# Performance work log

Hardware: AMD Instinct MI355X
Metric: run time of the kernel (lower is better)

The kernel has to match this reference:

```python
import jax, jax.numpy as jnp
import numpy as np

B, TQ, TK = 64, 1, 2048
QD, KD, U, H = 512, 512, 1024, 8
D = U // H  # per-head dim = 128


def setup_inputs() -> dict:
    key0 = jax.random.key(0)
    k0, k1, k2, k3, k4 = jax.random.split(key0, 5)
    query = jax.random.normal(k0, (B, TQ, QD), jnp.float32)
    key = jax.random.normal(k1, (B, TK, KD), jnp.float32)
    # 1x1 Conv1d == Linear: weight [out_ch, in_ch], bias [out_ch]
    Wq = jax.random.normal(k2, (U, QD), jnp.float32) / np.sqrt(QD).astype(np.float32)
    bq = jnp.zeros((U,), jnp.float32)
    Wk = jax.random.normal(k3, (U, KD), jnp.float32) / np.sqrt(KD).astype(np.float32)
    bk = jnp.zeros((U,), jnp.float32)
    # v is generated with torch.randn every forward in the original (unlearned);
    # here it is a fixed random vector of size D (per-head units).
    v = jax.random.normal(k4, (D,), jnp.float32)
    return {"query": query, "key": key, "Wq": Wq, "bq": bq, "Wk": Wk, "bk": bk, "v": v}


def reference(query, key, Wq, bq, Wk, bk, v):
    # 1x1 conv projections (channels-last linear)
    q = jnp.einsum('btq,uq->btu', query, Wq) + bq          # [B,TQ,U]
    k = jnp.einsum('btk,uk->btu', key, Wk) + bk            # [B,TK,U]
    # split heads: torch.stack(torch.split(x, D, dim=2), dim=1) -> [B,H,T,D]
    qs = q.reshape(B, TQ, H, D).transpose(0, 2, 1, 3)      # [B,H,TQ,D]
    ks = k.reshape(B, TK, H, D).transpose(0, 2, 1, 3)      # [B,H,TK,D]
    # weight-normalized random projection vector (b is zeros, folded away)
    g = np.float32(1.0) / np.sqrt(D).astype(np.float32)
    normed_v = g * v * jax.lax.rsqrt(jnp.sum(v * v))       # [D]
    # additive score: sum_d normed_v * tanh(ks + qs)  (qs broadcasts over TK)
    add = jnp.einsum('d,bhtd->bht', normed_v, jnp.tanh(ks + qs))  # [B,H,TK]
    # F.softmax without dim on a 4D tensor -> legacy dim=1 (heads axis)
    weights = jax.nn.softmax(add[:, :, None, :], axis=1)   # [B,H,TQ,TK]
    # value = unprojected key, shared across heads
    context = jnp.einsum('bhqt,btd->bhqd', weights, key)   # [B,H,TQ,KD]
    # view(B, TQ, -1): valid because TQ == 1
    return context.reshape(B, TQ, H * KD)
```

## Files before the change

kernel.cpp:

```cpp
#include <hip/hip_runtime.h>

#define B_   64
#define TK_  2048
#define KD_  512
#define U_   1024
#define H_   8
#define D_   128
#define MT   64
#define NTILE (TK_ / MT)
#define GRID (B_ * NTILE)

typedef float f32x4 __attribute__((ext_vector_type(4)));
typedef short short8 __attribute__((ext_vector_type(8)));

__device__ __forceinline__ short f2bf(float f) {
    unsigned u = __float_as_uint(f);
    u += 0x7fffu + ((u >> 16) & 1u);
    return (short)(u >> 16);
}
__device__ __forceinline__ float bf2f(short s) {
    return __uint_as_float(((unsigned)(unsigned short)s) << 16);
}
__device__ __forceinline__ float tanh_fast(float x) {
    float e = __builtin_amdgcn_exp2f(x * 2.885390081777927f);
    return 1.0f - 2.0f * __builtin_amdgcn_rcpf(1.0f + e);
}

__device__ __forceinline__ void wg_barrier_lds() {
    asm volatile("" ::: "memory");
    __builtin_amdgcn_s_waitcnt(0xC07F);
    __builtin_amdgcn_s_barrier();
    asm volatile("" ::: "memory");
}

__device__ __forceinline__ void write_frag(short* As, int t, int c4, float4 v) {
    int ks = c4 >> 5;
    int lq = (c4 >> 3) & 3;
    int E  = ((lq << 4) | (t & 15)) ^ (ks & 7);
    int si = ((ks * 4 + (t >> 4)) << 9) + (E << 3) + (c4 & 4);
    short4 h4;
    h4.x = f2bf(v.x); h4.y = f2bf(v.y); h4.z = f2bf(v.z); h4.w = f2bf(v.w);
    *(short4*)&As[si] = h4;
}

__global__ void nv_kernel(const float* __restrict__ v, float* __restrict__ wsNV) {
    __shared__ float red[D_];
    int tid = threadIdx.x;
    float x = v[tid];
    red[tid] = x * x;
    __syncthreads();
    if (tid == 0) {
        float s = 0.f;
        for (int i = 0; i < D_; ++i) s += red[i];
        red[0] = rsqrtf(s) * 0.08838834764831845f;
    }
    __syncthreads();
    wsNV[tid] = x * red[0];
}

__global__ void q_kernel(const float* __restrict__ query, const float* __restrict__ Wq,
                         const float* __restrict__ bq, const float* __restrict__ bk,
                         float* __restrict__ wsQ) {
    __shared__ float qrow[KD_];
    int b = blockIdx.x, ug = blockIdx.y, tid = threadIdx.x;
    if (tid < 128) ((float4*)qrow)[tid] = ((const float4*)(query + (size_t)b * KD_))[tid];
    __syncthreads();
    int u = ug * 256 + tid;
    const float4* wq = (const float4*)(Wq + (size_t)u * KD_);
    const float4* q4 = (const float4*)qrow;
    float acc = 0.f;
#pragma unroll 8
    for (int i = 0; i < KD_ / 4; ++i) {
        float4 a = q4[i], w = wq[i];
        acc += a.x * w.x + a.y * w.y + a.z * w.z + a.w * w.w;
    }
    wsQ[(size_t)b * U_ + u] = acc + bq[u] + bk[u];
}

__global__ void swz_kernel(const float* __restrict__ Wk, short* __restrict__ wsB) {
    int g = blockIdx.x * 256 + threadIdx.x;
    int slot = g >> 6, l = g & 63;
    int ublk = slot >> 4, ks = slot & 15;
    int u = ublk * 16 + (l & 15);
    int k0 = ks * 32 + ((l >> 4) << 3);
    const float* src = Wk + (size_t)u * KD_ + k0;
    short8 o;
#pragma unroll
    for (int j = 0; j < 8; ++j) o[j] = f2bf(src[j]);
    *(short8*)(wsB + (size_t)g * 8) = o;
}

template <bool ATOMIC>
__global__ __launch_bounds__(256, 2) void attn_kernel(
    const float* __restrict__ key, const short* __restrict__ wsB,
    const float* __restrict__ wsQ, const float* __restrict__ wsNV,
    float* __restrict__ outp)
{
    __shared__ short As[MT * KD_];
    __shared__ float S[MT][H_];
    __shared__ float Wt[MT][H_];

    int bx = blockIdx.x;
    int b = bx & 63, tt = bx >> 6;
    int tid = threadIdx.x;
    int w = tid >> 6, l = tid & 63;
    int l15 = l & 15;

    const float4* kt = (const float4*)(key + ((size_t)b * TK_ + (size_t)tt * MT) * KD_);

    float4 h0v[16], h1v[16];
#pragma unroll
    for (int j = 0; j < 16; ++j) {
        int idx = tid + j * 256;
        h0v[j] = kt[((idx >> 6) << 7) + (idx & 63)];
    }
#pragma unroll
    for (int j = 0; j < 16; ++j) {
        int idx = tid + j * 256;
        h1v[j] = kt[((idx >> 6) << 7) + (idx & 63) + 64];
    }
#pragma unroll
    for (int j = 0; j < 16; ++j) {
        int idx = tid + j * 256;
        write_frag(As, idx >> 6, (idx & 63) << 2, h0v[j]);
    }
    wg_barrier_lds();

    const short8* bp = (const short8*)wsB;

    float ps[4][4];
    f32x4 acc[4][4];
    short8 bc[4], bn[4];
    int bbase_cur = 0;

    for (int p = 0; p < 4; ++p) {
        int c = p >> 1, nh = p & 1;
        int ub = c * 512 + w * 128 + nh * 64;
        int bbase = (ub >> 4) * 1024 + l;
        bbase_cur = bbase;

        if (nh == 0) {
#pragma unroll
            for (int mf = 0; mf < 4; ++mf)
#pragma unroll
                for (int r = 0; r < 4; ++r) ps[mf][r] = 0.f;
        }
#pragma unroll
        for (int mf = 0; mf < 4; ++mf)
#pragma unroll
            for (int nf = 0; nf < 4; ++nf) acc[mf][nf] = (f32x4){0.f, 0.f, 0.f, 0.f};

#pragma unroll
        for (int nf = 0; nf < 4; ++nf) bc[nf] = bp[bbase + nf * 1024];

        auto gemm_seg = [&](int ks0, int ks1) {
#pragma unroll 1
            for (int ks = ks0; ks < ks1; ++ks) {
                if (ks < 15) {
#pragma unroll
                    for (int nf = 0; nf < 4; ++nf)
                        bn[nf] = bp[bbase_cur + nf * 1024 + (ks + 1) * 64];
                }
                int ab = ((ks * 4) << 9) + ((l ^ (ks & 7)) << 3);
                short8 a[4];
#pragma unroll
                for (int mf = 0; mf < 4; ++mf)
                    a[mf] = *(const short8*)&As[ab + (mf << 9)];
#pragma unroll
                for (int mf = 0; mf < 4; ++mf)
#pragma unroll
                    for (int nf = 0; nf < 4; ++nf)
                        acc[mf][nf] = __builtin_amdgcn_mfma_f32_16x16x32_bf16(
                            a[mf], bc[nf], acc[mf][nf], 0, 0, 0);
                if (ks < 15) {
#pragma unroll
                    for (int nf = 0; nf < 4; ++nf) bc[nf] = bn[nf];
                }
            }
        };

        if (p == 0) {
            gemm_seg(0, 8);
#pragma unroll
            for (int j = 0; j < 16; ++j) {
                int idx = tid + j * 256;
                write_frag(As, idx >> 6, ((idx & 63) << 2) + 256, h1v[j]);
            }
            wg_barrier_lds();
            gemm_seg(8, 16);
        } else {
            gemm_seg(0, 16);
        }

        float qv[4], nv[4];
#pragma unroll
        for (int nf = 0; nf < 4; ++nf) {
            qv[nf] = wsQ[(size_t)b * U_ + ub + nf * 16 + l15];
            nv[nf] = wsNV[nh * 64 + nf * 16 + l15];
        }
#pragma unroll
        for (int mf = 0; mf < 4; ++mf)
#pragma unroll
            for (int r = 0; r < 4; ++r) {
                float pp = ps[mf][r];
#pragma unroll
                for (int nf = 0; nf < 4; ++nf)
                    pp += nv[nf] * tanh_fast(acc[mf][nf][r] + qv[nf]);
                ps[mf][r] = pp;
            }
        if (nh == 1) {
            int h = c * 4 + w;
#pragma unroll
            for (int mf = 0; mf < 4; ++mf)
#pragma unroll
                for (int r = 0; r < 4; ++r) {
                    float pp = ps[mf][r];
                    pp += __shfl_xor(pp, 1);
                    pp += __shfl_xor(pp, 2);
                    pp += __shfl_xor(pp, 4);
                    pp += __shfl_xor(pp, 8);
                    if (l15 == 0) S[mf * 16 + (l >> 4) * 4 + r][h] = pp;
                }
        }
    }
    wg_barrier_lds();

    if (tid < MT) {
        float sv[H_];
        float mx = -1e30f;
#pragma unroll
        for (int h = 0; h < H_; ++h) { sv[h] = S[tid][h]; mx = fmaxf(mx, sv[h]); }
        float sum = 0.f;
#pragma unroll
        for (int h = 0; h < H_; ++h) {
            sv[h] = __builtin_amdgcn_exp2f((sv[h] - mx) * 1.4426950408889634f);
            sum += sv[h];
        }
        float inv = __builtin_amdgcn_rcpf(sum);
#pragma unroll
        for (int h = 0; h < H_; ++h) Wt[tid][h] = sv[h] * inv;
    }
    wg_barrier_lds();

    int dg8 = (tid & 63) << 3;
    int hp = tid >> 6;
    int vks = dg8 >> 5, vlq = (dg8 >> 3) & 3;
    float cacc[2][8] = {};
#pragma unroll 1
    for (int t = 0; t < MT; ++t) {
        int E = ((vlq << 4) | (t & 15)) ^ (vks & 7);
        short8 kk = *(const short8*)&As[((vks * 4 + (t >> 4)) << 9) + (E << 3)];
        float w0 = Wt[t][2 * hp], w1 = Wt[t][2 * hp + 1];
#pragma unroll
        for (int d = 0; d < 8; ++d) {
            float kv = bf2f(kk[d]);
            cacc[0][d] += w0 * kv;
            cacc[1][d] += w1 * kv;
        }
    }
    if (ATOMIC) {
        float* ob = outp + (size_t)b * (H_ * KD_);
#pragma unroll
        for (int j = 0; j < 2; ++j)
#pragma unroll
            for (int d = 0; d < 8; ++d)
                atomicAdd(&ob[(2 * hp + j) * KD_ + dg8 + d], cacc[j][d]);
    } else {
        float* pb = outp + (size_t)bx * (H_ * KD_);
#pragma unroll
        for (int j = 0; j < 2; ++j) {
            *(f32x4*)&pb[(2 * hp + j) * KD_ + dg8]     = *(f32x4*)&cacc[j][0];
            *(f32x4*)&pb[(2 * hp + j) * KD_ + dg8 + 4] = *(f32x4*)&cacc[j][4];
        }
    }
}

__global__ void reduce_kernel(const float* __restrict__ partial, float* __restrict__ out) {
    int o = blockIdx.x * 256 + threadIdx.x;
    int b = o >> 10;
    int u4 = o & 1023;
    const f32x4* p4 = (const f32x4*)partial;
    f32x4 s = {0.f, 0.f, 0.f, 0.f};
#pragma unroll 8
    for (int tt = 0; tt < NTILE; ++tt)
        s += p4[((size_t)(tt * 64 + b)) * 1024 + u4];
    ((f32x4*)out)[o] = s;
}

extern "C" void kernel_launch(void* const* d_in, const int* in_sizes, int n_in,
                              void* d_out, int out_size, void* d_ws, size_t ws_size,
                              hipStream_t stream) {
    const float* query = (const float*)d_in[0];
    const float* key   = (const float*)d_in[1];
    const float* Wq    = (const float*)d_in[2];
    const float* bq    = (const float*)d_in[3];
    const float* Wk    = (const float*)d_in[4];
    const float* bk    = (const float*)d_in[5];
    const float* v     = (const float*)d_in[6];
    float* out = (float*)d_out;

    char* ws = (char*)d_ws;
    float* wsNV = (float*)ws;
    float* wsQ  = (float*)(ws + 4096);
    short* wsB  = (short*)(ws + 524288);
    float* wsP  = (float*)(ws + 2 * 1024 * 1024);

    size_t need = 2 * 1024 * 1024 + (size_t)GRID * (H_ * KD_) * sizeof(float);

    nv_kernel<<<1, 128, 0, stream>>>(v, wsNV);
    q_kernel<<<dim3(64, 4), 256, 0, stream>>>(query, Wq, bq, bk, wsQ);
    swz_kernel<<<256, 256, 0, stream>>>(Wk, wsB);

    if (ws_size >= need) {
        attn_kernel<false><<<GRID, 256, 0, stream>>>(key, wsB, wsQ, wsNV, wsP);
        reduce_kernel<<<256, 256, 0, stream>>>(wsP, out);
    } else {
        hipMemsetAsync(d_out, 0, (size_t)out_size * sizeof(float), stream);
        attn_kernel<true><<<GRID, 256, 0, stream>>>(key, wsB, wsQ, wsNV, out);
    }
}
```

Before: 557.7 us.

## Use 512-thread blocks with one head per wave and padded LDS layout

Doubles the attention block to 8 waves so each wave owns one head's 128 projection units. The per-wave loop shrinks from four passes to two, cutting serial MFMA work per wave and raising occupancy. The swizzled LDS fragment layout is replaced by a row-major layout padded by 8 elements to limit bank conflicts, and the context accumulation now has each thread handle 4 columns. The trade-off is higher register pressure under launch_bounds(512,4) and possibly more LDS bank conflicts than the XOR swizzle had.

Measured after the change: 646.5 us. 1.16x slower.

```diff
diff --git a/kernel.cpp b/kernel.cpp
--- a/kernel.cpp
+++ b/kernel.cpp
@@ -7,6 +7,8 @@
 #define H_   8
 #define D_   128
 #define MT   64
+#define APAD 8
+#define ASTR (KD_ + APAD)
 #define NTILE (TK_ / MT)
 #define GRID (B_ * NTILE)
 
@@ -31,16 +33,6 @@
     __builtin_amdgcn_s_waitcnt(0xC07F);
     __builtin_amdgcn_s_barrier();
     asm volatile("" ::: "memory");
-}
-
-__device__ __forceinline__ void write_frag(short* As, int t, int c4, float4 v) {
-    int ks = c4 >> 5;
-    int lq = (c4 >> 3) & 3;
-    int E  = ((lq << 4) | (t & 15)) ^ (ks & 7);
-    int si = ((ks * 4 + (t >> 4)) << 9) + (E << 3) + (c4 & 4);
-    short4 h4;
-    h4.x = f2bf(v.x); h4.y = f2bf(v.y); h4.z = f2bf(v.z); h4.w = f2bf(v.w);
-    *(short4*)&As[si] = h4;
 }
 
 __global__ void nv_kernel(const float* __restrict__ v, float* __restrict__ wsNV) {
@@ -91,12 +83,12 @@
 }
 
 template <bool ATOMIC>
-__global__ __launch_bounds__(256, 2) void attn_kernel(
+__global__ __launch_bounds__(512, 4) void attn_kernel(
     const float* __restrict__ key, const short* __restrict__ wsB,
     const float* __restrict__ wsQ, const float* __restrict__ wsNV,
     float* __restrict__ outp)
 {
-    __shared__ short As[MT * KD_];
+    __shared__ short As[MT * ASTR];
     __shared__ float S[MT][H_];
     __shared__ float Wt[MT][H_];
 
@@ -104,25 +96,29 @@
     int b = bx & 63, tt = bx >> 6;
     int tid = threadIdx.x;
     int w = tid >> 6, l = tid & 63;
-    int l15 = l & 15;
+    int l15 = l & 15, lq = l >> 4;
 
     const float4* kt = (const float4*)(key + ((size_t)b * TK_ + (size_t)tt * MT) * KD_);
 
-    float4 h0v[16], h1v[16];
-#pragma unroll
-    for (int j = 0; j < 16; ++j) {
-        int idx = tid + j * 256;
+    float4 h0v[8], h1v[8];
+#pragma unroll
+    for (int j = 0; j < 8; ++j) {
+        int idx = tid + j * 512;
         h0v[j] = kt[((idx >> 6) << 7) + (idx & 63)];
     }
 #pragma unroll
-    for (int j = 0; j < 16; ++j) {
-        int idx = tid + j * 256;
+    for (int j = 0; j < 8; ++j) {
+        int idx = tid + j * 512;
         h1v[j] = kt[((idx >> 6) << 7) + (idx & 63) + 64];
     }
 #pragma unroll
-    for (int j = 0; j < 16; ++j) {
-        int idx = tid + j * 256;
-        write_frag(As, idx >> 6, (idx & 63) << 2, h0v[j]);
+    for (int j = 0; j < 8; ++j) {
+        int idx = tid + j * 512;
+        int t = idx >> 6, c4 = (idx & 63) << 2;
+        float4 v = h0v[j];
+        short4 h4;
+        h4.x = f2bf(v.x); h4.y = f2bf(v.y); h4.z = f2bf(v.z); h4.w = f2bf(v.w);
+        *(short4*)&As[t * ASTR + c4] = h4;
     }
     wg_barrier_lds();
 
@@ -133,22 +129,27 @@
     short8 bc[4], bn[4];
     int bbase_cur = 0;
 
-    for (int p = 0; p < 4; ++p) {
-        int c = p >> 1, nh = p & 1;
-        int ub = c * 512 + w * 128 + nh * 64;
+#pragma unroll
+    for (int mf = 0; mf < 4; ++mf)
+#pragma unroll
+        for (int r = 0; r < 4; ++r) ps[mf][r] = 0.f;
+
+    for (int p = 0; p < 2; ++p) {
+        int ub = w * 128 + p * 64;
         int bbase = (ub >> 4) * 1024 + l;
         bbase_cur = bbase;
 
-        if (nh == 0) {
-#pragma unroll
-            for (int mf = 0; mf < 4; ++mf)
-#pragma unroll
-                for (int r = 0; r < 4; ++r) ps[mf][r] = 0.f;
+#pragma unroll
+        for (int mf = 0; mf < 4; ++mf)
+#pragma unroll
+            for (int nf = 0; nf < 4; ++nf) acc[mf][nf] = (f32x4){0.f, 0.f, 0.f, 0.f};
+
+        float qv[4], nv[4];
+#pragma unroll
+        for (int nf = 0; nf < 4; ++nf) {
+            qv[nf] = wsQ[(size_t)b * U_ + ub + nf * 16 + l15];
+            nv[nf] = wsNV[p * 64 + nf * 16 + l15];
         }
-#pragma unroll
-        for (int mf = 0; mf < 4; ++mf)
-#pragma unroll
-            for (int nf = 0; nf < 4; ++nf) acc[mf][nf] = (f32x4){0.f, 0.f, 0.f, 0.f};
 
 #pragma unroll
         for (int nf = 0; nf < 4; ++nf) bc[nf] = bp[bbase + nf * 1024];
@@ -161,11 +162,10 @@
                     for (int nf = 0; nf < 4; ++nf)
                         bn[nf] = bp[bbase_cur + nf * 1024 + (ks + 1) * 64];
                 }
-                int ab = ((ks * 4) << 9) + ((l ^ (ks & 7)) << 3);
                 short8 a[4];
 #pragma unroll
                 for (int mf = 0; mf < 4; ++mf)
-                    a[mf] = *(const short8*)&As[ab + (mf << 9)];
+                    a[mf] = *(const short8*)&As[(mf * 16 + l15) * ASTR + ks * 32 + (lq << 3)];
 #pragma unroll
                 for (int mf = 0; mf < 4; ++mf)
 #pragma unroll
@@ -182,9 +182,13 @@
         if (p == 0) {
             gemm_seg(0, 8);
 #pragma unroll
-            for (int j = 0; j < 16; ++j) {
-                int idx = tid + j * 256;
-                write_frag(As, idx >> 6, ((idx & 63) << 2) + 256, h1v[j]);
+            for (int j = 0; j < 8; ++j) {
+                int idx = tid + j * 512;
+                int t = idx >> 6, c4 = ((idx & 63) << 2) + 256;
+                float4 v = h1v[j];
+                short4 h4;
+                h4.x = f2bf(v.x); h4.y = f2bf(v.y); h4.z = f2bf(v.z); h4.w = f2bf(v.w);
+                *(short4*)&As[t * ASTR + c4] = h4;
             }
             wg_barrier_lds();
             gemm_seg(8, 16);
@@ -192,12 +196,6 @@
             gemm_seg(0, 16);
         }
 
-        float qv[4], nv[4];
-#pragma unroll
-        for (int nf = 0; nf < 4; ++nf) {
-            qv[nf] = wsQ[(size_t)b * U_ + ub + nf * 16 + l15];
-            nv[nf] = wsNV[nh * 64 + nf * 16 + l15];
-        }
 #pragma unroll
         for (int mf = 0; mf < 4; ++mf)
 #pragma unroll
@@ -208,8 +206,7 @@
                     pp += nv[nf] * tanh_fast(acc[mf][nf][r] + qv[nf]);
                 ps[mf][r] = pp;
             }
-        if (nh == 1) {
-            int h = c * 4 + w;
+        if (p == 1) {
 #pragma unroll
             for (int mf = 0; mf < 4; ++mf)
 #pragma unroll
@@ -219,7 +216,7 @@
                     pp += __shfl_xor(pp, 2);
                     pp += __shfl_xor(pp, 4);
                     pp += __shfl_xor(pp, 8);
-                    if (l15 == 0) S[mf * 16 + (l >> 4) * 4 + r][h] = pp;
+                    if (l15 == 0) S[mf * 16 + lq * 4 + r][w] = pp;
                 }
         }
     }
@@ -242,36 +239,31 @@
     }
     wg_barrier_lds();
 
-    int dg8 = (tid & 63) << 3;
-    int hp = tid >> 6;
-    int vks = dg8 >> 5, vlq = (dg8 >> 3) & 3;
-    float cacc[2][8] = {};
+    int dg = (tid & 127) << 2;
+    int hp = tid >> 7;
+    float cacc[2][4] = {};
 #pragma unroll 1
     for (int t = 0; t < MT; ++t) {
-        int E = ((vlq << 4) | (t & 15)) ^ (vks & 7);
-        short8 kk = *(const short8*)&As[((vks * 4 + (t >> 4)) << 9) + (E << 3)];
+        short4 kk = *(const short4*)&As[t * ASTR + dg];
+        float k0 = bf2f(kk.x), k1 = bf2f(kk.y), k2 = bf2f(kk.z), k3 = bf2f(kk.w);
         float w0 = Wt[t][2 * hp], w1 = Wt[t][2 * hp + 1];
-#pragma unroll
-        for (int d = 0; d < 8; ++d) {
-            float kv = bf2f(kk[d]);
-            cacc[0][d] += w0 * kv;
-            cacc[1][d] += w1 * kv;
-        }
+        cacc[0][0] += w0 * k0; cacc[0][1] += w0 * k1;
+        cacc[0][2] += w0 * k2; cacc[0][3] += w0 * k3;
+        cacc[1][0] += w1 * k0; cacc[1][1] += w1 * k1;
+        cacc[1][2] += w1 * k2; cacc[1][3] += w1 * k3;
     }
     if (ATOMIC) {
         float* ob = outp + (size_t)b * (H_ * KD_);
 #pragma unroll
         for (int j = 0; j < 2; ++j)
 #pragma unroll
-            for (int d = 0; d < 8; ++d)
-                atomicAdd(&ob[(2 * hp + j) * KD_ + dg8 + d], cacc[j][d]);
+            for (int d = 0; d < 4; ++d)
+                atomicAdd(&ob[(2 * hp + j) * KD_ + dg + d], cacc[j][d]);
     } else {
         float* pb = outp + (size_t)bx * (H_ * KD_);
 #pragma unroll
-        for (int j = 0; j < 2; ++j) {
-            *(f32x4*)&pb[(2 * hp + j) * KD_ + dg8]     = *(f32x4*)&cacc[j][0];
-            *(f32x4*)&pb[(2 * hp + j) * KD_ + dg8 + 4] = *(f32x4*)&cacc[j][4];
-        }
+        for (int j = 0; j < 2; ++j)
+            *(f32x4*)&pb[(2 * hp + j) * KD_ + dg] = *(f32x4*)&cacc[j][0];
     }
 }
 
@@ -312,10 +304,10 @@
     swz_kernel<<<256, 256, 0, stream>>>(Wk, wsB);
 
     if (ws_size >= need) {
-        attn_kernel<false><<<GRID, 256, 0, stream>>>(key, wsB, wsQ, wsNV, wsP);
+        attn_kernel<false><<<GRID, 512, 0, stream>>>(key, wsB, wsQ, wsNV, wsP);
         reduce_kernel<<<256, 256, 0, stream>>>(wsP, out);
     } else {
         hipMemsetAsync(d_out, 0, (size_t)out_size * sizeof(float), stream);
-        attn_kernel<true><<<GRID, 256, 0, stream>>>(key, wsB, wsQ, wsNV, out);
-    }
-}
+        attn_kernel<true><<<GRID, 512, 0, stream>>>(key, wsB, wsQ, wsNV, out);
+    }
+}
```
